# Kernel tuning notes

Measured on AMD Instinct MI355X. Metric: run time of the kernel, lower is better.

## Reference

```python
import jax, jax.numpy as jnp
import numpy as np

B, K_LEN, Q_LEN, E, H = 16, 2048, 1024, 512, 8


def _layer_norm(x, g, b, eps=1e-5):
    mu = jnp.mean(x, axis=-1, keepdims=True)
    var = jnp.mean(jnp.square(x - mu), axis=-1, keepdims=True)
    return (x - mu) * jax.lax.rsqrt(var + eps) * g + b


def setup_inputs() -> dict:
    key = jax.random.key(0)
    ks = jax.random.split(key, 8)
    w = lambda k, sh: (jax.random.normal(k, sh, dtype=jnp.float32) * 0.02)
    return {
        "x_key": jax.random.normal(ks[0], (B, K_LEN, E), dtype=jnp.float32),
        "in_proj_w": w(ks[1], (3 * E, E)),
        "in_proj_b": jnp.zeros((3 * E,), jnp.float32),
        "out_w": w(ks[2], (E, E)),
        "out_b": jnp.zeros((E,), jnp.float32),
        "ln1_g": jnp.ones((E,), jnp.float32),
        "ln1_b": jnp.zeros((E,), jnp.float32),
        "w1": w(ks[3], (E, E)),
        "b1": jnp.zeros((E,), jnp.float32),
        "w2": w(ks[4], (E, E)),
        "b2": jnp.zeros((E,), jnp.float32),
        "ln2_g": jnp.ones((E,), jnp.float32),
        "ln2_b": jnp.zeros((E,), jnp.float32),
        "query_length": Q_LEN,
        "key_padding_mask": jax.random.bernoulli(ks[5], 0.2, (B, K_LEN)),
    }


def _attn_mask(key_length, query_length, key_padding_mask):
    # True = masked.  triu causal part, shared across batch/heads.
    triu = jnp.triu(jnp.ones((key_length, key_length), dtype=bool), k=1)
    m = triu[-query_length:]  # [Q, K]
    m = m[None] | key_padding_mask[:, None, :]  # [B, Q, K]
    not_eye = ~jnp.eye(key_length, dtype=bool)[-query_length:]  # [Q, K]
    m = m & not_eye[None]  # diagonal (self) always attendable
    return m  # [B, Q, K]; identical across heads


def reference(x_key, in_proj_w, in_proj_b, out_w, out_b,
              ln1_g, ln1_b, w1, b1, w2, b2, ln2_g, ln2_b,
              query_length, key_padding_mask):
    b, k_len, e = x_key.shape
    dh = e // H
    q_len = query_length

    # pad key_padding_mask on the left with its first column (static shapes)
    L = key_padding_mask.shape[1]
    if L < k_len:
        pad = jnp.repeat(key_padding_mask[:, :1], k_len - L, axis=1)
        key_padding_mask = jnp.concatenate([pad, key_padding_mask], axis=1)

    query = x_key[:, -q_len:]  # [B, Q, E]

    wq, wk, wv = jnp.split(in_proj_w, 3, axis=0)
    bq, bk, bv = jnp.split(in_proj_b, 3, axis=0)
    q = (query @ wq.T + bq).reshape(b, q_len, H, dh).transpose(0, 2, 1, 3)
    k = (x_key @ wk.T + bk).reshape(b, k_len, H, dh).transpose(0, 2, 1, 3)
    v = (x_key @ wv.T + bv).reshape(b, k_len, H, dh).transpose(0, 2, 1, 3)

    scores = jnp.einsum('bhqd,bhkd->bhqk', q, k) * (dh ** -0.5)
    mask = _attn_mask(k_len, q_len, key_padding_mask)  # [B, Q, K]
    scores = jnp.where(mask[:, None], -jnp.inf, scores)
    attn = jax.nn.softmax(scores, axis=-1)  # [B, H, Q, K]

    ctx = jnp.einsum('bhqk,bhkd->bhqd', attn, v)
    ctx = ctx.transpose(0, 2, 1, 3).reshape(b, q_len, e)
    attn_out = ctx @ out_w.T + out_b

    t = _layer_norm(attn_out + query, ln1_g, ln1_b)
    ff = jax.nn.relu(t @ w1.T + b1) @ w2.T + b2
    output = _layer_norm(ff + t, ln2_g, ln2_b)
    attn_weights = attn.mean(axis=1)  # head-averaged, torch default
    return output, attn_weights
```

## Files before the change

kernel.cpp:

```cpp
#include <hip/hip_runtime.h>

typedef unsigned short u16t;
typedef __attribute__((ext_vector_type(4))) unsigned short us4;
typedef __attribute__((ext_vector_type(8))) unsigned short us8;
typedef __attribute__((ext_vector_type(8))) short s8v;
typedef __attribute__((ext_vector_type(4))) float f4v;

#define NB 16
#define KL 2048
#define QL 1024
#define EE 512
#define NH 8
#define DH 64

#define QSCALE 0.18033688011112042f
#define SENT (-60000.0f)

__device__ __forceinline__ float b2f(u16t u) {
  return __uint_as_float(((unsigned)u) << 16);
}
__device__ __forceinline__ u16t f2b(float f) {
  unsigned u = __float_as_uint(f);
  u += 0x7fffu + ((u >> 16) & 1u);
  return (u16t)(u >> 16);
}
__device__ __forceinline__ u16t f2b_fast(float f) {
  return (u16t)((__float_as_uint(f) + 0x8000u) >> 16);
}
__device__ __forceinline__ float fexp2(float x) {
  return __builtin_amdgcn_exp2f(x);
}

__device__ __forceinline__ int detect_mode(const int* kpm_i) {
  bool small = true, oddzero = true, evenone = false;
  for (int i = 0; i < 64; ++i) {
    unsigned v = (unsigned)kpm_i[i];
    if (v > 1u) small = false;
    if ((i & 1) && v != 0u) oddzero = false;
    if (!(i & 1) && v == 1u) evenone = true;
  }
  return !small ? 0 : ((oddzero && evenone) ? 2 : 1);
}

__global__ __launch_bounds__(256) void cvt_weights(
    const float* __restrict__ wi, const float* __restrict__ wo,
    const float* __restrict__ wf1, const float* __restrict__ wf2,
    u16t* __restrict__ dst) {
  int i = blockIdx.x * 256 + threadIdx.x;
  const float* src;
  int j;
  if (i < 196608) { src = wi; j = i; }
  else if (i < 262144) { src = wo; j = i - 196608; }
  else if (i < 327680) { src = wf1; j = i - 262144; }
  else { src = wf2; j = i - 327680; }
  float4 v = ((const float4*)src)[j];
  us4 o = {f2b(v.x), f2b(v.y), f2b(v.z), f2b(v.w)};
  *(us4*)&dst[i * 4] = o;
}

__global__ __launch_bounds__(256) void mfma_gemm_qkv(
    const float* __restrict__ A, const u16t* __restrict__ Wb,
    const float* __restrict__ bias, u16t* __restrict__ q_ws,
    u16t* __restrict__ k_ws, u16t* __restrict__ v_ws) {
  const int Kd = EE;
  __shared__ u16t Alds[128 * 40];
  __shared__ u16t Blds[128 * 40];
  const int t = threadIdx.x;
  const int n0 = blockIdx.x * 128, m0 = blockIdx.y * 128;
  const int lane = t & 63, w = t >> 6;
  const int col = lane & 15, quad = lane >> 4;
  const int wm = w & 1, wn = w >> 1;

  const int arow = t >> 1, ahalf = t & 1;
  const int wrow = t >> 1, wseg = t & 1;

  f4v acc[4][4] = {};

  for (int kc = 0; kc < Kd; kc += 32) {
    const float* ap = &A[(size_t)(m0 + arow) * Kd + kc + ahalf * 16];
    float4 f0 = ((const float4*)ap)[0];
    float4 f1 = ((const float4*)ap)[1];
    float4 f2_ = ((const float4*)ap)[2];
    float4 f3 = ((const float4*)ap)[3];
    const u16t* wp = &Wb[(size_t)(n0 + wrow) * Kd + kc + wseg * 16];
    us8 w0 = *(const us8*)wp;
    us8 w1 = *(const us8*)(wp + 8);
    __syncthreads();
    us8 o0 = {f2b(f0.x), f2b(f0.y), f2b(f0.z), f2b(f0.w),
              f2b(f1.x), f2b(f1.y), f2b(f1.z), f2b(f1.w)};
    us8 o1 = {f2b(f2_.x), f2b(f2_.y), f2b(f2_.z), f2b(f2_.w),
              f2b(f3.x), f2b(f3.y), f2b(f3.z), f2b(f3.w)};
    *(us8*)&Alds[arow * 40 + ahalf * 16] = o0;
    *(us8*)&Alds[arow * 40 + ahalf * 16 + 8] = o1;
    *(us8*)&Blds[wrow * 40 + wseg * 16] = w0;
    *(us8*)&Blds[wrow * 40 + wseg * 16 + 8] = w1;
    __syncthreads();
    s8v af[4], bf[4];
#pragma unroll
    for (int mt = 0; mt < 4; ++mt)
      af[mt] = *(s8v*)&Alds[(wm * 64 + mt * 16 + col) * 40 + quad * 8];
#pragma unroll
    for (int nt = 0; nt < 4; ++nt)
      bf[nt] = *(s8v*)&Blds[(wn * 64 + nt * 16 + col) * 40 + quad * 8];
#pragma unroll
    for (int mt = 0; mt < 4; ++mt)
#pragma unroll
      for (int nt = 0; nt < 4; ++nt)
        acc[mt][nt] = __builtin_amdgcn_mfma_f32_16x16x32_bf16(
            af[mt], bf[nt], acc[mt][nt], 0, 0, 0);
  }

  float bv[4];
#pragma unroll
  for (int nt = 0; nt < 4; ++nt) bv[nt] = bias[n0 + wn * 64 + nt * 16 + col];

#pragma unroll
  for (int nt = 0; nt < 4; ++nt) {
    int n = n0 + wn * 64 + nt * 16 + col;
    int sec = n >> 9, hh = (n >> 6) & 7, dd = n & 63;
#pragma unroll
    for (int mt = 0; mt < 4; ++mt)
#pragma unroll
      for (int r = 0; r < 4; ++r) {
        int m = m0 + wm * 64 + mt * 16 + quad * 4 + r;
        int bb_ = m >> 11, pos = m & 2047;
        float val = acc[mt][nt][r] + bv[nt];
        if (sec == 0) {
          if (pos >= QL)
            q_ws[((bb_ * NH + hh) * QL + pos - QL) * DH + dd] =
                f2b(val * QSCALE);
        } else if (sec == 1) {
          k_ws[((bb_ * NH + hh) * KL + pos) * DH + dd] = f2b(val);
        } else {
          v_ws[((bb_ * NH + hh) * DH + dd) * KL + pos] = f2b(val);
        }
      }
  }
}

__global__ __launch_bounds__(256) void mfma_gemm_bias(
    const u16t* __restrict__ A, const u16t* __restrict__ Wb,
    const float* __restrict__ bias, u16t* __restrict__ C, int M, int N,
    int Kd, int relu) {
  __shared__ u16t Alds[128 * 40];
  __shared__ u16t Blds[128 * 40];
  const int t = threadIdx.x;
  const int n0 = blockIdx.x * 128, m0 = blockIdx.y * 128;
  const int lane = t & 63, w = t >> 6;
  const int col = lane & 15, quad = lane >> 4;
  const int wm = w & 1, wn = w >> 1;
  const int row = t >> 1, seg = t & 1;

  f4v acc[4][4] = {};

  for (int kc = 0; kc < Kd; kc += 32) {
    const u16t* ap = &A[(size_t)(m0 + row) * Kd + kc + seg * 16];
    us8 a0 = *(const us8*)ap;
    us8 a1 = *(const us8*)(ap + 8);
    const u16t* wp = &Wb[(size_t)(n0 + row) * Kd + kc + seg * 16];
    us8 w0 = *(const us8*)wp;
    us8 w1 = *(const us8*)(wp + 8);
    __syncthreads();
    *(us8*)&Alds[row * 40 + seg * 16] = a0;
    *(us8*)&Alds[row * 40 + seg * 16 + 8] = a1;
    *(us8*)&Blds[row * 40 + seg * 16] = w0;
    *(us8*)&Blds[row * 40 + seg * 16 + 8] = w1;
    __syncthreads();
    s8v af[4], bf[4];
#pragma unroll
    for (int mt = 0; mt < 4; ++mt)
      af[mt] = *(s8v*)&Alds[(wm * 64 + mt * 16 + col) * 40 + quad * 8];
#pragma unroll
    for (int nt = 0; nt < 4; ++nt)
      bf[nt] = *(s8v*)&Blds[(wn * 64 + nt * 16 + col) * 40 + quad * 8];
#pragma unroll
    for (int mt = 0; mt < 4; ++mt)
#pragma unroll
      for (int nt = 0; nt < 4; ++nt)
        acc[mt][nt] = __builtin_amdgcn_mfma_f32_16x16x32_bf16(
            af[mt], bf[nt], acc[mt][nt], 0, 0, 0);
  }

  float bv[4];
#pragma unroll
  for (int nt = 0; nt < 4; ++nt) bv[nt] = bias[n0 + wn * 64 + nt * 16 + col];

#pragma unroll
  for (int mt = 0; mt < 4; ++mt)
#pragma unroll
    for (int nt = 0; nt < 4; ++nt) {
      int n = n0 + wn * 64 + nt * 16 + col;
#pragma unroll
      for (int r = 0; r < 4; ++r) {
        int m = m0 + wm * 64 + mt * 16 + quad * 4 + r;
        float v = acc[mt][nt][r] + bv[nt];
        if (relu) v = fmaxf(v, 0.f);
        C[(size_t)m * N + n] = f2b(v);
      }
    }
}

__global__ __launch_bounds__(256, 2) void attn_fwd(
    const u16t* __restrict__ qw, const u16t* __restrict__ kw,
    const u16t* __restrict__ vw, const int* kpm_i, const unsigned char* kpm_b,
    u16t* __restrict__ ctx_out, float* __restrict__ m_ws,
    float* __restrict__ l_ws) {
  const int q0 = blockIdx.x * 32;
  const int bh = blockIdx.y;
  const int b = bh >> 3, h = bh & 7;
  const int t = threadIdx.x;
  const int lane = t & 63, w = t >> 6;
  const int col = lane & 15, quad = lane >> 4;

  __shared__ unsigned char padb[KL];
  __shared__ __align__(16) char ubuf[32768];
  u16t (*plds)[2][16][72] = (u16t (*)[2][16][72])ubuf;
  float (*ctxm)[32][64] = (float (*)[32][64])ubuf;
  __shared__ float mlm[4][2][32];
  __shared__ float Lrow[32], ewf[4][32];
  __shared__ int mode_s;

  if (t == 0) mode_s = detect_mode(kpm_i);
  __syncthreads();
  const int mode = mode_s;
  for (int i = t; i < KL; i += 256) {
    int idx = b * KL + i;
    padb[i] = (mode == 0)
                  ? (kpm_b[idx] != 0)
                  : (mode == 1 ? (kpm_i[idx] != 0) : (kpm_i[2 * idx] != 0));
  }
  __syncthreads();

  s8v qa[2][2];
#pragma unroll
  for (int st = 0; st < 2; ++st)
#pragma unroll
    for (int hf = 0; hf < 2; ++hf)
      qa[st][hf] = *(const s8v*)&qw[(bh * QL + q0 + st * 16 + col) * DH +
                                    quad * 8 + 32 * hf];

  const f4v zf = {0.f, 0.f, 0.f, 0.f};
  const s8v ones = {16256, 16256, 16256, 16256,
                    16256, 16256, 16256, 16256};

  f4v cacc[2][4];
  f4v lacc[2];
#pragma unroll
  for (int st = 0; st < 2; ++st) {
    lacc[st] = zf;
#pragma unroll
    for (int dt = 0; dt < 4; ++dt) cacc[st][dt] = zf;
  }
  float mr[2][4];
#pragma unroll
  for (int st = 0; st < 2; ++st)
#pragma unroll
    for (int r = 0; r < 4; ++r) mr[st][r] = SENT;

  const int qmaxk = q0 + 31 + QL;
  const size_t kbase = (size_t)bh * KL * DH;
  const size_t vbase = (size_t)bh * DH * KL;

  int kc = w * 64;
  s8v kcur[4][2];
#pragma unroll
  for (int tt = 0; tt < 4; ++tt) {
    const u16t* kp = &kw[kbase + (size_t)(kc + tt * 16 + col) * DH + quad * 8];
    kcur[tt][0] = *(const s8v*)kp;
    kcur[tt][1] = *(const s8v*)(kp + 32);
  }

  while (true) {
    s8v vcur[4][2];
#pragma unroll
    for (int dt = 0; dt < 4; ++dt) {
      const u16t* vp = &vw[vbase + (size_t)(dt * 16 + col) * KL + kc + quad * 8];
      vcur[dt][0] = *(const s8v*)vp;
      vcur[dt][1] = *(const s8v*)(vp + 32);
    }
    const int kcn = kc + 256;
    const bool more = (kcn <= qmaxk);
    s8v knxt[4][2];
    if (more) {
#pragma unroll
      for (int tt = 0; tt < 4; ++tt) {
        const u16t* kp =
            &kw[kbase + (size_t)(kcn + tt * 16 + col) * DH + quad * 8];
        knxt[tt][0] = *(const s8v*)kp;
        knxt[tt][1] = *(const s8v*)(kp + 32);
      }
    }

    f4v sts[2][4];
#pragma unroll
    for (int tt = 0; tt < 4; ++tt)
#pragma unroll
      for (int st = 0; st < 2; ++st) {
        f4v c = __builtin_amdgcn_mfma_f32_16x16x32_bf16(qa[st][0],
                                                        kcur[tt][0], zf, 0, 0, 0);
        sts[st][tt] = __builtin_amdgcn_mfma_f32_16x16x32_bf16(
            qa[st][1], kcur[tt][1], c, 0, 0, 0);
      }

    const bool interior = (kc + 63 < q0 + QL);

#pragma unroll
    for (int st = 0; st < 2; ++st) {
      float cmax[4] = {SENT, SENT, SENT, SENT};
      if (interior) {
#pragma unroll
        for (int tt = 0; tt < 4; ++tt) {
          bool pad = padb[kc + tt * 16 + col] != 0;
#pragma unroll
          for (int r = 0; r < 4; ++r) {
            float v = pad ? -1.0e30f : sts[st][tt][r];
            sts[st][tt][r] = v;
            cmax[r] = fmaxf(cmax[r], v);
          }
        }
      } else {
#pragma unroll
        for (int tt = 0; tt < 4; ++tt) {
          int key = kc + tt * 16 + col;
          bool pad = padb[key] != 0;
#pragma unroll
          for (int r = 0; r < 4; ++r) {
            int qrow = q0 + st * 16 + quad * 4 + r;
            bool al = (key <= qrow + QL) && (!pad || key == qrow + QL);
            float v = al ? sts[st][tt][r] : -1.0e30f;
            sts[st][tt][r] = v;
            cmax[r] = fmaxf(cmax[r], v);
          }
        }
      }
#pragma unroll
      for (int mk = 1; mk < 16; mk <<= 1)
#pragma unroll
        for (int r = 0; r < 4; ++r)
          cmax[r] = fmaxf(cmax[r], __shfl_xor(cmax[r], mk, 16));
      float alpha[4];
#pragma unroll
      for (int r = 0; r < 4; ++r) {
        float mn = fmaxf(mr[st][r], cmax[r]);
        alpha[r] = fexp2(mr[st][r] - mn);
        mr[st][r] = mn;
      }
#pragma unroll
      for (int r = 0; r < 4; ++r) {
        lacc[st][r] *= alpha[r];
#pragma unroll
        for (int dt = 0; dt < 4; ++dt) cacc[st][dt][r] *= alpha[r];
      }
#pragma unroll
      for (int tt = 0; tt < 4; ++tt)
#pragma unroll
        for (int r = 0; r < 4; ++r) {
          float p = fexp2(sts[st][tt][r] - mr[st][r]);
          plds[w][st][quad * 4 + r][tt * 16 + col] = f2b_fast(p);
        }
    }

    s8v pa[2][2];
#pragma unroll
    for (int st = 0; st < 2; ++st)
#pragma unroll
      for (int hf = 0; hf < 2; ++hf)
        pa[st][hf] = *(const s8v*)&plds[w][st][col][hf * 32 + quad * 8];
#pragma unroll
    for (int st = 0; st < 2; ++st) {
      lacc[st] = __builtin_amdgcn_mfma_f32_16x16x32_bf16(pa[st][0], ones,
                                                         lacc[st], 0, 0, 0);
      lacc[st] = __builtin_amdgcn_mfma_f32_16x16x32_bf16(pa[st][1], ones,
                                                         lacc[st], 0, 0, 0);
    }
#pragma unroll
    for (int dt = 0; dt < 4; ++dt)
#pragma unroll
      for (int st = 0; st < 2; ++st) {
        cacc[st][dt] = __builtin_amdgcn_mfma_f32_16x16x32_bf16(
            pa[st][0], vcur[dt][0], cacc[st][dt], 0, 0, 0);
        cacc[st][dt] = __builtin_amdgcn_mfma_f32_16x16x32_bf16(
            pa[st][1], vcur[dt][1], cacc[st][dt], 0, 0, 0);
      }

    if (!more) break;
    kc = kcn;
#pragma unroll
    for (int tt = 0; tt < 4; ++tt) {
      kcur[tt][0] = knxt[tt][0];
      kcur[tt][1] = knxt[tt][1];
    }
  }

  __syncthreads();
#pragma unroll
  for (int st = 0; st < 2; ++st)
#pragma unroll
    for (int dt = 0; dt < 4; ++dt)
#pragma unroll
      for (int r = 0; r < 4; ++r)
        ctxm[w][st * 16 + quad * 4 + r][dt * 16 + col] = cacc[st][dt][r];
  if (col == 0) {
#pragma unroll
    for (int st = 0; st < 2; ++st)
#pragma unroll
      for (int r = 0; r < 4; ++r) {
        mlm[w][0][st * 16 + quad * 4 + r] = mr[st][r];
        mlm[w][1][st * 16 + quad * 4 + r] = lacc[st][r];
      }
  }
  __syncthreads();
  if (t < 32) {
    int q = t;
    float M = mlm[0][0][q];
#pragma unroll
    for (int ww = 1; ww < 4; ++ww) M = fmaxf(M, mlm[ww][0][q]);
    float L = 0.f;
#pragma unroll
    for (int ww = 0; ww < 4; ++ww) {
      float e = fexp2(mlm[ww][0][q] - M);
      ewf[ww][q] = e;
      L += mlm[ww][1][q] * e;
    }
    Lrow[q] = 1.0f / L;
    m_ws[bh * QL + q0 + q] = M;
    l_ws[bh * QL + q0 + q] = L;
  }
  __syncthreads();
  for (int i = t; i < 2048; i += 256) {
    int q = i >> 6, d = i & 63;
    float v = ctxm[0][q][d] * ewf[0][q] + ctxm[1][q][d] * ewf[1][q] +
              ctxm[2][q][d] * ewf[2][q] + ctxm[3][q][d] * ewf[3][q];
    v *= Lrow[q];
    ctx_out[(b * QL + q0 + q) * EE + h * DH + d] = f2b(v);
  }
}

__global__ __launch_bounds__(256) void attn_aw(
    const u16t* __restrict__ qw, const u16t* __restrict__ kw,
    const int* kpm_i, const unsigned char* kpm_b,
    const float* __restrict__ m_ws, const float* __restrict__ l_ws,
    float* __restrict__ aw_out) {
  const int q0 = blockIdx.x * 32;
  const int k0 = blockIdx.y * 128;
  const int b = blockIdx.z;
  const int t = threadIdx.x;
  const int lane = t & 63, w = t >> 6;
  const int col = lane & 15, quad = lane >> 4;
  const int qmaxk = q0 + 31 + QL;

  if (k0 > qmaxk) {
    for (int i = t; i < 32 * 128; i += 256) {
      int q = i >> 7, c = i & 127;
      aw_out[(b * QL + q0 + q) * KL + k0 + c] = 0.f;
    }
    return;
  }

  __shared__ unsigned char padb[128];
  __shared__ int mode_s;
  if (t == 0) mode_s = detect_mode(kpm_i);
  __syncthreads();
  const int mode = mode_s;
  if (t < 128) {
    int idx = b * KL + k0 + t;
    padb[t] = (mode == 0)
                  ? (kpm_b[idx] != 0)
                  : (mode == 1 ? (kpm_i[idx] != 0) : (kpm_i[2 * idx] != 0));
  }
  __syncthreads();

  const bool interior = (k0 + 127 < q0 + QL);

  const int kt = k0 + w * 32;
  const f4v zf = {0.f, 0.f, 0.f, 0.f};
  f4v acc[2][2];
#pragma unroll
  for (int st = 0; st < 2; ++st)
#pragma unroll
    for (int tt = 0; tt < 2; ++tt) acc[st][tt] = zf;

  for (int h = 0; h < NH; ++h) {
    const int bh = b * NH + h;
    s8v qa[2][2];
#pragma unroll
    for (int st = 0; st < 2; ++st)
#pragma unroll
      for (int hf = 0; hf < 2; ++hf)
        qa[st][hf] = *(const s8v*)&qw[(bh * QL + q0 + st * 16 + col) * DH +
                                      quad * 8 + 32 * hf];
    float Mv[2][4], Li[2][4];
#pragma unroll
    for (int st = 0; st < 2; ++st)
#pragma unroll
      for (int r = 0; r < 4; ++r) {
        int q = q0 + st * 16 + quad * 4 + r;
        Mv[st][r] = m_ws[bh * QL + q];
        Li[st][r] = 1.0f / l_ws[bh * QL + q];
      }
#pragma unroll
    for (int tt = 0; tt < 2; ++tt) {
      const int ktt = kt + tt * 16;
      if (ktt > qmaxk) continue;
      const u16t* kp = &kw[(bh * KL + ktt + col) * DH + quad * 8];
      s8v kb0 = *(const s8v*)kp;
      s8v kb1 = *(const s8v*)(kp + 32);
      int key = ktt + col;
      bool pad = padb[key - k0] != 0;
#pragma unroll
      for (int st = 0; st < 2; ++st) {
        f4v c = __builtin_amdgcn_mfma_f32_16x16x32_bf16(qa[st][0], kb0, zf, 0, 0, 0);
        c = __builtin_amdgcn_mfma_f32_16x16x32_bf16(qa[st][1], kb1, c, 0, 0, 0);
        if (interior) {
#pragma unroll
          for (int r = 0; r < 4; ++r) {
            float p = pad ? 0.f : fexp2(c[r] - Mv[st][r]) * Li[st][r];
            acc[st][tt][r] += 0.125f * p;
          }
        } else {
#pragma unroll
          for (int r = 0; r < 4; ++r) {
            int qrow = q0 + st * 16 + quad * 4 + r;
            bool al = (key <= qrow + QL) && (!pad || key == qrow + QL);
            float p = al ? fexp2(c[r] - Mv[st][r]) * Li[st][r] : 0.f;
            acc[st][tt][r] += 0.125f * p;
          }
        }
      }
    }
  }
#pragma unroll
  for (int st = 0; st < 2; ++st)
#pragma unroll
    for (int tt = 0; tt < 2; ++tt)
#pragma unroll
      for (int r = 0; r < 4; ++r)
        aw_out[(b * QL + q0 + st * 16 + quad * 4 + r) * KL + kt + tt * 16 +
               col] = acc[st][tt][r];
}

__global__ __launch_bounds__(256) void ln_res(
    const u16t* __restrict__ x, const u16t* __restrict__ res_b,
    const float* __restrict__ res_f, int res_is_xkey,
    const float* __restrict__ g, const float* __restrict__ bb,
    u16t* __restrict__ out_b, float* __restrict__ out_f, int out_f32) {
  __shared__ float red[4];
  int row = blockIdx.x;
  int t = threadIdx.x;
  int base = row * EE;
  float r0, r1;
  if (res_is_xkey) {
    int b = row >> 10, qq = row & 1023;
    int rbase = (b * KL + QL + qq) * EE;
    r0 = res_f[rbase + t];
    r1 = res_f[rbase + t + 256];
  } else {
    r0 = b2f(res_b[base + t]);
    r1 = b2f(res_b[base + t + 256]);
  }
  float a0 = b2f(x[base + t]) + r0;
  float a1 = b2f(x[base + t + 256]) + r1;
  float sv = a0 + a1;
#pragma unroll
  for (int off = 32; off > 0; off >>= 1) sv += __shfl_down(sv, off);
  if ((t & 63) == 0) red[t >> 6] = sv;
  __syncthreads();
  float mu = (red[0] + red[1] + red[2] + red[3]) * (1.0f / 512.0f);
  __syncthreads();
  float d0 = a0 - mu, d1 = a1 - mu;
  float vv = d0 * d0 + d1 * d1;
#pragma unroll
  for (int off = 32; off > 0; off >>= 1) vv += __shfl_down(vv, off);
  if ((t & 63) == 0) red[t >> 6] = vv;
  __syncthreads();
  float var = (red[0] + red[1] + red[2] + red[3]) * (1.0f / 512.0f);
  float rs = rsqrtf(fmaxf(var, 0.f) + 1e-5f);
  float o0 = d0 * rs * g[t] + bb[t];
  float o1 = d1 * rs * g[t + 256] + bb[t + 256];
  if (out_f32) {
    out_f[base + t] = o0;
    out_f[base + t + 256] = o1;
  } else {
    out_b[base + t] = f2b(o0);
    out_b[base + t + 256] = f2b(o1);
  }
}

extern "C" void kernel_launch(void* const* d_in, const int* in_sizes, int n_in,
                              void* d_out, int out_size, void* d_ws,
                              size_t ws_size, hipStream_t stream) {
  const float* x_key = (const float*)d_in[0];
  const float* in_proj_w = (const float*)d_in[1];
  const float* in_proj_b = (const float*)d_in[2];
  const float* out_w = (const float*)d_in[3];
  const float* out_b = (const float*)d_in[4];
  const float* ln1_g = (const float*)d_in[5];
  const float* ln1_b = (const float*)d_in[6];
  const float* w1 = (const float*)d_in[7];
  const float* b1 = (const float*)d_in[8];
  const float* w2 = (const float*)d_in[9];
  const float* b2 = (const float*)d_in[10];
  const float* ln2_g = (const float*)d_in[11];
  const float* ln2_b = (const float*)d_in[12];
  const void* kpm = d_in[14];

  float* out = (float*)d_out;
  u16t* ws = (u16t*)d_ws;

  u16t* wb_inproj = ws;
  u16t* wb_out = ws + 786432;
  u16t* wb_w1 = ws + 1048576;
  u16t* wb_w2 = ws + 1310720;
  u16t* q_ws = ws + 1572864;
  u16t* k_ws = ws + 9961472;
  u16t* v_ws = ws + 26738688;
  u16t* ctx_ws = ws + 43515904;
  float* m_ws = (float*)(ws + 51904512);
  float* l_ws = m_ws + 131072;
  u16t* ao_ws = q_ws;
  u16t* t_ws = ctx_ws;
  u16t* h1_ws = k_ws;
  u16t* ff_ws = v_ws;
  float* aw_out = out + (NB * QL * EE);

  cvt_weights<<<1536, 256, 0, stream>>>(in_proj_w, out_w, w1, w2, wb_inproj);
  mfma_gemm_qkv<<<dim3(12, 256), 256, 0, stream>>>(x_key, wb_inproj,
                                                   in_proj_b, q_ws, k_ws,
                                                   v_ws);
  attn_fwd<<<dim3(QL / 32, NB * NH), 256, 0, stream>>>(
      q_ws, k_ws, v_ws, (const int*)kpm, (const unsigned char*)kpm, ctx_ws,
      m_ws, l_ws);
  attn_aw<<<dim3(QL / 32, KL / 128, NB), 256, 0, stream>>>(
      q_ws, k_ws, (const int*)kpm, (const unsigned char*)kpm, m_ws, l_ws,
      aw_out);
  mfma_gemm_bias<<<dim3(4, 128), 256, 0, stream>>>(ctx_ws, wb_out, out_b,
                                                   ao_ws, NB * QL, EE, EE, 0);
  ln_res<<<NB * QL, 256, 0, stream>>>(ao_ws, nullptr, x_key, 1, ln1_g, ln1_b,
                                      t_ws, nullptr, 0);
  mfma_gemm_bias<<<dim3(4, 128), 256, 0, stream>>>(t_ws, wb_w1, b1, h1_ws,
                                                   NB * QL, EE, EE, 1);
  mfma_gemm_bias<<<dim3(4, 128), 256, 0, stream>>>(h1_ws, wb_w2, b2, ff_ws,
                                                   NB * QL, EE, EE, 0);
  ln_res<<<NB * QL, 256, 0, stream>>>(ff_ws, t_ws, nullptr, 0, ln2_g, ln2_b,
                                      nullptr, out, 1);
}
```

Before: 974.5 us.

## Double-buffer per-head fragment loads in attention-weights kernel and precompute scaled inverse sum

```diff
diff --git a/kernel.cpp b/kernel.cpp
--- a/kernel.cpp
+++ b/kernel.cpp
@@ -422,9 +422,10 @@
       ewf[ww][q] = e;
       L += mlm[ww][1][q] * e;
     }
-    Lrow[q] = 1.0f / L;
+    float inv = 1.0f / L;
+    Lrow[q] = inv;
     m_ws[bh * QL + q0 + q] = M;
-    l_ws[bh * QL + q0 + q] = L;
+    l_ws[bh * QL + q0 + q] = 0.125f * inv;
   }
   __syncthreads();
   for (int i = t; i < 2048; i += 256) {
@@ -436,7 +437,7 @@
   }
 }
 
-__global__ __launch_bounds__(256) void attn_aw(
+__global__ __launch_bounds__(256, 2) void attn_aw(
     const u16t* __restrict__ qw, const u16t* __restrict__ kw,
     const int* kpm_i, const unsigned char* kpm_b,
     const float* __restrict__ m_ws, const float* __restrict__ l_ws,
@@ -480,55 +481,88 @@
 #pragma unroll
     for (int tt = 0; tt < 2; ++tt) acc[st][tt] = zf;
 
-  for (int h = 0; h < NH; ++h) {
-    const int bh = b * NH + h;
-    s8v qa[2][2];
+  bool padl[2];
+  padl[0] = padb[kt + col - k0] != 0;
+  padl[1] = padb[kt + 16 + col - k0] != 0;
+
+  auto load_frags = [&](int hh, s8v qa[2][2], s8v kb[2][2]) {
+    const int bh = b * NH + hh;
 #pragma unroll
     for (int st = 0; st < 2; ++st)
 #pragma unroll
       for (int hf = 0; hf < 2; ++hf)
         qa[st][hf] = *(const s8v*)&qw[(bh * QL + q0 + st * 16 + col) * DH +
                                       quad * 8 + 32 * hf];
-    float Mv[2][4], Li[2][4];
-#pragma unroll
-    for (int st = 0; st < 2; ++st)
-#pragma unroll
-      for (int r = 0; r < 4; ++r) {
-        int q = q0 + st * 16 + quad * 4 + r;
-        Mv[st][r] = m_ws[bh * QL + q];
-        Li[st][r] = 1.0f / l_ws[bh * QL + q];
-      }
+#pragma unroll
+    for (int tt = 0; tt < 2; ++tt) {
+      const u16t* kp = &kw[((size_t)bh * KL + kt + tt * 16 + col) * DH +
+                           quad * 8];
+      kb[tt][0] = *(const s8v*)kp;
+      kb[tt][1] = *(const s8v*)(kp + 32);
+    }
+  };
+  auto load_ml = [&](int hh, float Mv[2][4], float Li[2][4]) {
+    const int bh = b * NH + hh;
+#pragma unroll
+    for (int st = 0; st < 2; ++st) {
+      float4 m4 = *(const float4*)&m_ws[bh * QL + q0 + st * 16 + quad * 4];
+      float4 l4 = *(const float4*)&l_ws[bh * QL + q0 + st * 16 + quad * 4];
+      Mv[st][0] = m4.x; Mv[st][1] = m4.y; Mv[st][2] = m4.z; Mv[st][3] = m4.w;
+      Li[st][0] = l4.x; Li[st][1] = l4.y; Li[st][2] = l4.z; Li[st][3] = l4.w;
+    }
+  };
+  auto compute = [&](const s8v qa[2][2], const s8v kb[2][2],
+                     const float Mv[2][4], const float Li[2][4]) {
 #pragma unroll
     for (int tt = 0; tt < 2; ++tt) {
       const int ktt = kt + tt * 16;
       if (ktt > qmaxk) continue;
-      const u16t* kp = &kw[(bh * KL + ktt + col) * DH + quad * 8];
-      s8v kb0 = *(const s8v*)kp;
-      s8v kb1 = *(const s8v*)(kp + 32);
-      int key = ktt + col;
-      bool pad = padb[key - k0] != 0;
+      const bool pad = padl[tt];
+      const int key = ktt + col;
 #pragma unroll
       for (int st = 0; st < 2; ++st) {
-        f4v c = __builtin_amdgcn_mfma_f32_16x16x32_bf16(qa[st][0], kb0, zf, 0, 0, 0);
-        c = __builtin_amdgcn_mfma_f32_16x16x32_bf16(qa[st][1], kb1, c, 0, 0, 0);
+        f4v c = __builtin_amdgcn_mfma_f32_16x16x32_bf16(qa[st][0], kb[tt][0],
+                                                        zf, 0, 0, 0);
+        c = __builtin_amdgcn_mfma_f32_16x16x32_bf16(qa[st][1], kb[tt][1], c,
+                                                    0, 0, 0);
         if (interior) {
 #pragma unroll
           for (int r = 0; r < 4; ++r) {
-            float p = pad ? 0.f : fexp2(c[r] - Mv[st][r]) * Li[st][r];
-            acc[st][tt][r] += 0.125f * p;
+            float e = fexp2(c[r] - Mv[st][r]);
+            float li = pad ? 0.f : Li[st][r];
+            acc[st][tt][r] = fmaf(e, li, acc[st][tt][r]);
           }
         } else {
 #pragma unroll
           for (int r = 0; r < 4; ++r) {
             int qrow = q0 + st * 16 + quad * 4 + r;
             bool al = (key <= qrow + QL) && (!pad || key == qrow + QL);
-            float p = al ? fexp2(c[r] - Mv[st][r]) * Li[st][r] : 0.f;
-            acc[st][tt][r] += 0.125f * p;
+            float e = fexp2(c[r] - Mv[st][r]);
+            float li = al ? Li[st][r] : 0.f;
+            acc[st][tt][r] = fmaf(e, li, acc[st][tt][r]);
           }
         }
       }
     }
-  }
+  };
+
+  s8v qaA[2][2], kbA[2][2], qaB[2][2], kbB[2][2];
+  float MvA[2][4], LiA[2][4], MvB[2][4], LiB[2][4];
+
+  load_frags(0, qaA, kbA);
+  load_ml(0, MvA, LiA);
+#pragma unroll
+  for (int hp = 0; hp < NH; hp += 2) {
+    load_frags(hp + 1, qaB, kbB);
+    load_ml(hp + 1, MvB, LiB);
+    compute(qaA, kbA, MvA, LiA);
+    if (hp + 2 < NH) {
+      load_frags(hp + 2, qaA, kbA);
+      load_ml(hp + 2, MvA, LiA);
+    }
+    compute(qaB, kbB, MvB, LiB);
+  }
+
 #pragma unroll
   for (int st = 0; st < 2; ++st)
 #pragma unroll
```

Result: no change. 970.4 us (-0.4%).
